# Kernel optimization log

Measured on AMD Instinct MI355X. Metric: run time of the kernel, lower is better.

The kernel has to match this reference:

```python
import jax, jax.numpy as jnp
import numpy as np

PS = 2      # patch_size
TOPK = 3    # topk


def setup_inputs() -> dict:
    key = jax.random.key(0)
    x = jax.random.normal(key, (16, 128, 64, 64), dtype=jnp.float32)
    alpha = jnp.asarray(5.0, dtype=jnp.float32)
    return {"x": x, "alpha": alpha}


def reference(x, alpha):
    ps = PS
    b, c, h, w = x.shape
    nph, npw = h // ps, w // ps
    npatch = nph * npw
    pa = ps * ps
    # F.normalize(x, p=2, dim=-3): L2-normalize over channels
    nrm = jnp.sqrt(jnp.sum(x * x, axis=1, keepdims=True))
    x = x / jnp.maximum(nrm, 1e-12)
    # patchify: [b,c,h,w] -> [b,c,num_patches,patch_area]
    x = x.reshape(b * c * nph, ps, npw, ps)
    x = jnp.swapaxes(x, 1, 2).reshape(b, c, npatch, pa)
    diag = np.arange(ps) * (ps + 1)          # diagonal positions within a patch
    x = x[:, :, :, diag]                     # [b,c,npatch,ps]
    x = jnp.swapaxes(x, 1, 3)                # [b,ps,npatch,c]
    # per-diagonal-pixel patch correlation matrix
    corr = jnp.einsum('bpnc,bpmc->bpnm', x, x)           # [b,ps,np,np]
    avg = jnp.mean(corr, axis=1, keepdims=True)
    corr = jnp.concatenate([corr, avg], axis=1)          # [b,ps+1,np,np]
    # gaussian self-suppression mask (1 - gaussian centered at each patch)
    rat_s = 0.05
    sr, sc = nph * rat_s, npw * rat_s
    ind_r = jnp.arange(nph, dtype=jnp.float32).reshape(1, nph, 1)
    ind_c = jnp.arange(npw, dtype=jnp.float32).reshape(1, 1, npw)
    cr, cc = jnp.meshgrid(jnp.arange(nph, dtype=jnp.float32),
                          jnp.arange(npw, dtype=jnp.float32), indexing='ij')
    cent_r = cr.reshape(npatch, 1, 1)
    cent_c = cc.reshape(npatch, 1, 1)
    g = jnp.exp(-(ind_r - cent_r) ** 2 / (2.0 * sr * sr)) \
        * jnp.exp(-(ind_c - cent_c) ** 2 / (2.0 * sc * sc))   # [np,nph,npw]
    mask = (1.0 - g).reshape(1, 1, npatch, npatch)
    s = (corr * mask) * alpha
    # dual (row + column) softmax
    a = jax.nn.softmax(s, axis=-1) * jax.nn.softmax(s, axis=-2)  # [b,ps+1,np,np]
    # scatter: diagonal in-patch pixels get their own map, rest get the avg map
    src = np.full(pa, ps, dtype=np.int64)
    src[diag] = np.arange(ps)
    a = a[:, src]                              # [b,pa,np,np]
    # un-patchify attention back to [b, npatch, h, w]
    a = jnp.swapaxes(a, 1, 3)                  # [b,np,np,pa]
    a = a.reshape(b * npatch * nph, npw, ps, ps)
    a = jnp.swapaxes(a, 1, 2)
    a = a.reshape(b, npatch, h, w)
    # top-k over the patch (correlation-source) dim
    vals = jax.lax.top_k(jnp.moveaxis(a, 1, -1), TOPK)[0]  # [b,h,w,k]
    return jnp.moveaxis(vals, -1, 1)           # [b,k,h,w]
```

## Files before the change

kernel.cpp:

```cpp
#include <hip/hip_runtime.h>
#include <math.h>

#define NB 16
#define NCH 128
#define NH 64
#define NW 64
#define NP 1024

#define TN 32
#define TM 128
#define KC 32
#define KP 36
#define PK 40

#define NTILE 144

typedef __attribute__((ext_vector_type(8))) short short8v;
typedef __attribute__((ext_vector_type(4))) float f32x4;

__device__ __forceinline__ float med3(float a, float b, float c) {
  return __builtin_amdgcn_fmed3f(a, b, c);
}
__device__ __forceinline__ void top3_ins(float& t0, float& t1, float& t2, float a) {
  float n0 = fmaxf(t0, a);
  float n1 = med3(a, t0, t1);
  float n2 = med3(a, t1, t2);
  t0 = n0; t1 = n1; t2 = n2;
}
__device__ __forceinline__ float dot4(float4 a, float4 b) {
  return a.x * b.x + a.y * b.y + a.z * b.z + a.w * b.w;
}
__device__ __forceinline__ ushort f2bf(float f) {
  unsigned u = __float_as_uint(f);
  unsigned r = (u + 0x7FFFu + ((u >> 16) & 1u)) >> 16;
  return (ushort)r;
}
__device__ __forceinline__ float bf2f(ushort h) {
  return __uint_as_float(((unsigned)h) << 16);
}

__global__ __launch_bounds__(256) void prep_split(const float* __restrict__ x,
                                                  ushort* __restrict__ Vs,
                                                  float* __restrict__ rsum) {
  int blk = blockIdx.x;
  int t = threadIdx.x;
  int gid = blk * 256 + t;
  if (gid < NB * 3 * NP) rsum[gid] = 0.f;

  int b = blk >> 5;
  int c = (blk >> 4) & 1;
  int ng = blk & 15;
  int nl = t >> 2;
  int kq = t & 3;
  int n = ng * 64 + nl;
  int i = 2 * (n >> 5) + c;
  int j = 2 * (n & 31) + c;
  const float* xp = x + (size_t)b * NCH * NH * NW + i * NW + j;

  float v[32];
#pragma unroll
  for (int e = 0; e < 32; ++e)
    v[e] = xp[(size_t)(kq * 32 + e) * NH * NW];

  float ss = 0.f;
#pragma unroll
  for (int e = 0; e < 32; ++e) ss += v[e] * v[e];
  ss += __shfl_xor(ss, 1, 64);
  ss += __shfl_xor(ss, 2, 64);
  float r = 1.0f / fmaxf(sqrtf(ss), 1e-12f);

  size_t base = ((size_t)(b * 2 + c) * 3) * NP * NCH + (size_t)n * NCH + kq * 32;
  ushort* p1 = Vs + base;
  ushort* p2 = Vs + base + (size_t)NP * NCH;
  ushort* p3 = Vs + base + (size_t)2 * NP * NCH;
#pragma unroll
  for (int kg2 = 0; kg2 < 4; ++kg2) {
    ushort h1[8], h2[8], h3[8];
#pragma unroll
    for (int e = 0; e < 8; ++e) {
      float vv = v[kg2 * 8 + e] * r;
      ushort a = f2bf(vv);
      float r1 = vv - bf2f(a);
      ushort bq = f2bf(r1);
      float r2 = r1 - bf2f(bq);
      ushort cq = f2bf(r2);
      h1[e] = a; h2[e] = bq; h3[e] = cq;
    }
    *(float4*)(p1 + kg2 * 8) = *(float4*)h1;
    *(float4*)(p2 + kg2 * 8) = *(float4*)h2;
    *(float4*)(p3 + kg2 * 8) = *(float4*)h3;
  }
}

__global__ __launch_bounds__(256, 4) void gemm_mfma(
    const ushort* __restrict__ Vs, const float* __restrict__ alpha_p,
    float2* __restrict__ Sbuf, float* __restrict__ rsum) {
  __shared__ __align__(16) char smem[3 * 32 * PK * 2 + 3 * 128 * PK * 2];
  ushort (*A_s)[32][PK] = reinterpret_cast<ushort(*)[32][PK]>(smem);
  ushort (*B_s)[128][PK] =
      reinterpret_cast<ushort(*)[128][PK]>(smem + 3 * 32 * PK * 2);
  float2 (*Ts)[33] = reinterpret_cast<float2(*)[33]>(smem);

  int wg = blockIdx.x;
  int xcd = wg & 7;
  int jj = wg >> 3;
  int half = (jj >= NTILE) ? 1 : 0;
  const int b = 2 * xcd + half;
  int id = jj - half * NTILE;
  int g = 0;
  while (id >= 4 * (8 - g)) { id -= 4 * (8 - g); ++g; }
  const int ni = 4 * g + id / (8 - g);
  const int mj = g + id % (8 - g);
  const int n0 = ni * TN;
  const int m0 = mj * TM;

  const int t = threadIdx.x;
  const int lane = t & 63, wv = t >> 6;
  const int jc = lane & 15, kg = lane >> 4;
  const float alpha = *alpha_p;
  const ushort* Vsb = Vs + (size_t)b * 6 * NP * NCH;
  float* rs = rsum + (size_t)b * 3 * NP;

  f32x4 acc[2][2][2];
#pragma unroll
  for (int c = 0; c < 2; ++c)
#pragma unroll
    for (int i = 0; i < 2; ++i)
#pragma unroll
      for (int j = 0; j < 2; ++j) acc[c][i][j] = (f32x4){0.f, 0.f, 0.f, 0.f};

#pragma unroll
  for (int c = 0; c < 2; ++c) {
    for (int k0 = 0; k0 < NCH; k0 += KC) {
      __syncthreads();
#pragma unroll
      for (int q = 0; q < 2; ++q) {
        int flat = q * 256 + t;
        if (flat < 384) {
          int p = flat >> 7;
          int rem = flat & 127;
          int row = rem >> 2, u = rem & 3;
          const ushort* src = Vsb + ((size_t)(c * 3 + p) * NP + n0 + row) * NCH + k0 + u * 8;
          *(float4*)&A_s[p][row][u * 8] = *(const float4*)src;
        }
      }
#pragma unroll
      for (int q = 0; q < 6; ++q) {
        int flat = q * 256 + t;
        int p = flat >> 9;
        int rem = flat & 511;
        int row = rem >> 2, u = rem & 3;
        const ushort* src = Vsb + ((size_t)(c * 3 + p) * NP + m0 + row) * NCH + k0 + u * 8;
        *(float4*)&B_s[p][row][u * 8] = *(const float4*)src;
      }
      __syncthreads();

      short8v a1n0 = *(const short8v*)&A_s[0][jc][kg * 8];
      short8v a1n1 = *(const short8v*)&A_s[0][16 + jc][kg * 8];
      short8v a2n0 = *(const short8v*)&A_s[1][jc][kg * 8];
      short8v a2n1 = *(const short8v*)&A_s[1][16 + jc][kg * 8];
      short8v a3n0 = *(const short8v*)&A_s[2][jc][kg * 8];
      short8v a3n1 = *(const short8v*)&A_s[2][16 + jc][kg * 8];
      {
        short8v b0 = *(const short8v*)&B_s[0][wv * 32 + jc][kg * 8];
        short8v b1 = *(const short8v*)&B_s[0][wv * 32 + 16 + jc][kg * 8];
        acc[c][0][0] = __builtin_amdgcn_mfma_f32_16x16x32_bf16(a1n0, b0, acc[c][0][0], 0, 0, 0);
        acc[c][1][0] = __builtin_amdgcn_mfma_f32_16x16x32_bf16(a1n1, b0, acc[c][1][0], 0, 0, 0);
        acc[c][0][1] = __builtin_amdgcn_mfma_f32_16x16x32_bf16(a1n0, b1, acc[c][0][1], 0, 0, 0);
        acc[c][1][1] = __builtin_amdgcn_mfma_f32_16x16x32_bf16(a1n1, b1, acc[c][1][1], 0, 0, 0);
        acc[c][0][0] = __builtin_amdgcn_mfma_f32_16x16x32_bf16(a2n0, b0, acc[c][0][0], 0, 0, 0);
        acc[c][1][0] = __builtin_amdgcn_mfma_f32_16x16x32_bf16(a2n1, b0, acc[c][1][0], 0, 0, 0);
        acc[c][0][1] = __builtin_amdgcn_mfma_f32_16x16x32_bf16(a2n0, b1, acc[c][0][1], 0, 0, 0);
        acc[c][1][1] = __builtin_amdgcn_mfma_f32_16x16x32_bf16(a2n1, b1, acc[c][1][1], 0, 0, 0);
        acc[c][0][0] = __builtin_amdgcn_mfma_f32_16x16x32_bf16(a3n0, b0, acc[c][0][0], 0, 0, 0);
        acc[c][1][0] = __builtin_amdgcn_mfma_f32_16x16x32_bf16(a3n1, b0, acc[c][1][0], 0, 0, 0);
        acc[c][0][1] = __builtin_amdgcn_mfma_f32_16x16x32_bf16(a3n0, b1, acc[c][0][1], 0, 0, 0);
        acc[c][1][1] = __builtin_amdgcn_mfma_f32_16x16x32_bf16(a3n1, b1, acc[c][1][1], 0, 0, 0);
      }
      {
        short8v b0 = *(const short8v*)&B_s[1][wv * 32 + jc][kg * 8];
        short8v b1 = *(const short8v*)&B_s[1][wv * 32 + 16 + jc][kg * 8];
        acc[c][0][0] = __builtin_amdgcn_mfma_f32_16x16x32_bf16(a1n0, b0, acc[c][0][0], 0, 0, 0);
        acc[c][1][0] = __builtin_amdgcn_mfma_f32_16x16x32_bf16(a1n1, b0, acc[c][1][0], 0, 0, 0);
        acc[c][0][1] = __builtin_amdgcn_mfma_f32_16x16x32_bf16(a1n0, b1, acc[c][0][1], 0, 0, 0);
        acc[c][1][1] = __builtin_amdgcn_mfma_f32_16x16x32_bf16(a1n1, b1, acc[c][1][1], 0, 0, 0);
        acc[c][0][0] = __builtin_amdgcn_mfma_f32_16x16x32_bf16(a2n0, b0, acc[c][0][0], 0, 0, 0);
        acc[c][1][0] = __builtin_amdgcn_mfma_f32_16x16x32_bf16(a2n1, b0, acc[c][1][0], 0, 0, 0);
        acc[c][0][1] = __builtin_amdgcn_mfma_f32_16x16x32_bf16(a2n0, b1, acc[c][0][1], 0, 0, 0);
        acc[c][1][1] = __builtin_amdgcn_mfma_f32_16x16x32_bf16(a2n1, b1, acc[c][1][1], 0, 0, 0);
      }
      {
        short8v b0 = *(const short8v*)&B_s[2][wv * 32 + jc][kg * 8];
        short8v b1 = *(const short8v*)&B_s[2][wv * 32 + 16 + jc][kg * 8];
        acc[c][0][0] = __builtin_amdgcn_mfma_f32_16x16x32_bf16(a1n0, b0, acc[c][0][0], 0, 0, 0);
        acc[c][1][0] = __builtin_amdgcn_mfma_f32_16x16x32_bf16(a1n1, b0, acc[c][1][0], 0, 0, 0);
        acc[c][0][1] = __builtin_amdgcn_mfma_f32_16x16x32_bf16(a1n0, b1, acc[c][0][1], 0, 0, 0);
        acc[c][1][1] = __builtin_amdgcn_mfma_f32_16x16x32_bf16(a1n1, b1, acc[c][1][1], 0, 0, 0);
      }
    }
  }

  __syncthreads();
  float e[2][4][3];
#pragma unroll
  for (int ns = 0; ns < 2; ++ns)
#pragma unroll
    for (int r = 0; r < 4; ++r)
#pragma unroll
      for (int c = 0; c < 3; ++c) e[ns][r][c] = 0.f;

#pragma unroll
  for (int ns = 0; ns < 2; ++ns) {
#pragma unroll
    for (int r = 0; r < 4; ++r) {
      int nl = ns * 16 + kg * 4 + r;
      int n = n0 + nl;
      int nr = n >> 5, nc = n & 31;
      float2* rowp = Sbuf + ((size_t)b * NP + n) * NP;
#pragma unroll
      for (int ms = 0; ms < 2; ++ms) {
        int ml = wv * 32 + ms * 16 + jc;
        int m = m0 + ml;
        int dr = nr - (m >> 5);
        int dc = nc - (m & 31);
        float gss = __expf(-(float)(dr * dr + dc * dc) * 0.1953125f);
        float wgt = (1.0f - gss) * alpha;
        float2 sv = make_float2(acc[0][ns][ms][r] * wgt, acc[1][ns][ms][r] * wgt);
        Ts[ml][nl] = sv;
        if (m >= n) {
          rowp[m] = sv;
          e[ns][r][0] += __expf(sv.x);
          e[ns][r][1] += __expf(sv.y);
          e[ns][r][2] += __expf(0.5f * (sv.x + sv.y));
        }
      }
    }
  }
#pragma unroll
  for (int off = 1; off < 16; off <<= 1) {
#pragma unroll
    for (int ns = 0; ns < 2; ++ns)
#pragma unroll
      for (int r = 0; r < 4; ++r)
#pragma unroll
        for (int c = 0; c < 3; ++c)
          e[ns][r][c] += __shfl_xor(e[ns][r][c], off, 64);
  }
  if (jc == 0) {
#pragma unroll
    for (int ns = 0; ns < 2; ++ns)
#pragma unroll
      for (int r = 0; r < 4; ++r)
#pragma unroll
        for (int c = 0; c < 3; ++c)
          atomicAdd(&rs[(size_t)c * NP + (n0 + ns * 16 + kg * 4 + r)], e[ns][r][c]);
  }

  __syncthreads();
#pragma unroll
  for (int q = 0; q < 16; ++q) {
    int flat = q * 256 + t;
    int ml = flat >> 5;
    int r = flat & 31;
    int m = m0 + ml;
    int n = n0 + r;
    if (m > n) Sbuf[((size_t)b * NP + m) * NP + n] = Ts[ml][r];
  }
  {
    int ml = t >> 1;
    int rh = (t & 1) * 16;
    int m = m0 + ml;
    float e0 = 0.f, e1 = 0.f, e2 = 0.f;
#pragma unroll
    for (int rr = 0; rr < 16; ++rr) {
      int r = rh + rr;
      int n = n0 + r;
      float2 sv = Ts[ml][r];
      if (m > n) {
        e0 += __expf(sv.x);
        e1 += __expf(sv.y);
        e2 += __expf(0.5f * (sv.x + sv.y));
      }
    }
    e0 += __shfl_xor(e0, 1, 64);
    e1 += __shfl_xor(e1, 1, 64);
    e2 += __shfl_xor(e2, 1, 64);
    if ((t & 1) == 0) {
      atomicAdd(&rs[(size_t)0 * NP + m], e0);
      atomicAdd(&rs[(size_t)1 * NP + m], e1);
      atomicAdd(&rs[(size_t)2 * NP + m], e2);
    }
  }
}

__global__ __launch_bounds__(256) void recip_kernel(float* __restrict__ p, int nelem) {
  int i = blockIdx.x * 256 + threadIdx.x;
  if (i < nelem) p[i] = 1.0f / p[i];
}

__global__ __launch_bounds__(256, 4) void topk_kernel(
    const float2* __restrict__ Sbuf, const float* __restrict__ rinv,
    float* __restrict__ out) {
  const int n = blockIdx.x, b = blockIdx.y;
  const int t = threadIdx.x;
  const float* rb = rinv + (size_t)b * 3 * NP;
  float rin[3];
#pragma unroll
  for (int c = 0; c < 3; ++c) rin[c] = rb[c * NP + n];
  const float2* row = Sbuf + ((size_t)b * NP + n) * NP;

  float t0[3] = {0.f, 0.f, 0.f}, t1[3] = {0.f, 0.f, 0.f}, t2[3] = {0.f, 0.f, 0.f};
#pragma unroll
  for (int q = 0; q < 4; ++q) {
    int m = t + q * 256;
    float2 s01 = row[m];
    float s[3];
    s[0] = s01.x; s[1] = s01.y; s[2] = 0.5f * (s01.x + s01.y);
#pragma unroll
    for (int c = 0; c < 3; ++c) {
      float a = __expf(2.0f * s[c]) * rin[c] * rb[c * NP + m];
      top3_ins(t0[c], t1[c], t2[c], a);
    }
  }
#pragma unroll
  for (int off = 1; off < 64; off <<= 1) {
#pragma unroll
    for (int c = 0; c < 3; ++c) {
      float o0 = __shfl_xor(t0[c], off, 64);
      float o1 = __shfl_xor(t1[c], off, 64);
      float o2 = __shfl_xor(t2[c], off, 64);
      top3_ins(t0[c], t1[c], t2[c], o0);
      top3_ins(t0[c], t1[c], t2[c], o1);
      top3_ins(t0[c], t1[c], t2[c], o2);
    }
  }
  __shared__ float lds[4][9];
  if ((t & 63) == 0) {
    int w = t >> 6;
#pragma unroll
    for (int c = 0; c < 3; ++c) {
      lds[w][c * 3 + 0] = t0[c];
      lds[w][c * 3 + 1] = t1[c];
      lds[w][c * 3 + 2] = t2[c];
    }
  }
  __syncthreads();
  if (t == 0) {
#pragma unroll
    for (int w = 1; w < 4; ++w)
#pragma unroll
      for (int c = 0; c < 3; ++c) {
        top3_ins(t0[c], t1[c], t2[c], lds[w][c * 3 + 0]);
        top3_ins(t0[c], t1[c], t2[c], lds[w][c * 3 + 1]);
        top3_ins(t0[c], t1[c], t2[c], lds[w][c * 3 + 2]);
      }
    int pr = n >> 5, pc = n & 31;
#pragma unroll
    for (int c = 0; c < 3; ++c) {
      int ii0, jj0, ii1 = -1, jj1 = -1;
      if (c == 0)      { ii0 = 2 * pr;     jj0 = 2 * pc; }
      else if (c == 1) { ii0 = 2 * pr + 1; jj0 = 2 * pc + 1; }
      else             { ii0 = 2 * pr;     jj0 = 2 * pc + 1;
                         ii1 = 2 * pr + 1; jj1 = 2 * pc; }
      out[(((size_t)b * 3 + 0) * NH + ii0) * NW + jj0] = t0[c];
      out[(((size_t)b * 3 + 1) * NH + ii0) * NW + jj0] = t1[c];
      out[(((size_t)b * 3 + 2) * NH + ii0) * NW + jj0] = t2[c];
      if (ii1 >= 0) {
        out[(((size_t)b * 3 + 0) * NH + ii1) * NW + jj1] = t0[c];
        out[(((size_t)b * 3 + 1) * NH + ii1) * NW + jj1] = t1[c];
        out[(((size_t)b * 3 + 2) * NH + ii1) * NW + jj1] = t2[c];
      }
    }
  }
}

__global__ __launch_bounds__(256) void prep_kernel(const float* __restrict__ x,
                                                   float* __restrict__ V) {
  int blk = blockIdx.x;
  int t = threadIdx.x;
  int b = blk >> 3;
  int c = (blk >> 2) & 1;
  int n = (blk & 3) * 256 + t;
  int i = 2 * (n >> 5) + c;
  int j = 2 * (n & 31) + c;
  const float* xp = x + (size_t)b * NCH * NH * NW + i * NW + j;
  float ss = 0.f;
#pragma unroll 8
  for (int ch = 0; ch < NCH; ++ch) {
    float v = xp[(size_t)ch * NH * NW];
    ss += v * v;
  }
  float r = 1.0f / fmaxf(sqrtf(ss), 1e-12f);
  float* vp = V + (((size_t)b * 2 + c) * NP + n) * NCH;
#pragma unroll 8
  for (int ch = 0; ch < NCH; ++ch) {
    vp[ch] = xp[(size_t)ch * NH * NW] * r;
  }
}

template <int PASS>
__global__ __launch_bounds__(256, 2) void corr_kernel(
    const float* __restrict__ V, const float* __restrict__ alpha_p,
    float* __restrict__ rsum_g, float* __restrict__ out) {
  __shared__ __align__(16) float As[2][TN][KP];
  __shared__ __align__(16) float Bs[2][TM][KP];

  const int b = blockIdx.y;
  const int n0 = blockIdx.x * TN;
  const int t = threadIdx.x;
  const int tx = t & 31;
  const int ty = t >> 5;
  const float alpha = *alpha_p;
  const float* Vb = V + (size_t)b * 2 * NP * NCH;

  float sm[3][4];
  float t0[3][4], t1[3][4], t2[3][4];
  float rin[3][4];
#pragma unroll
  for (int c = 0; c < 3; ++c)
#pragma unroll
    for (int i = 0; i < 4; ++i) {
      sm[c][i] = 0.f;
      t0[c][i] = 0.f; t1[c][i] = 0.f; t2[c][i] = 0.f;
    }
  if (PASS == 2) {
#pragma unroll
    for (int c = 0; c < 3; ++c)
#pragma unroll
      for (int i = 0; i < 4; ++i) {
        int n = n0 + ty * 4 + i;
        rin[c][i] = 1.0f / rsum_g[((size_t)b * 3 + c) * NP + n];
      }
  }

  for (int mc = 0; mc < NP / TM; ++mc) {
    const int m0 = mc * TM;
    float acc[2][4][4];
#pragma unroll
    for (int c = 0; c < 2; ++c)
#pragma unroll
      for (int i = 0; i < 4; ++i)
#pragma unroll
        for (int j = 0; j < 4; ++j) acc[c][i][j] = 0.f;

    for (int k0 = 0; k0 < NCH; k0 += KC) {
      __syncthreads();
#pragma unroll
      for (int q = 0; q < 2; ++q) {
        int flat = q * 256 + t;
        int c = flat >> 8;
        int rem = flat & 255;
        int row = rem >> 3;
        int kgx = rem & 7;
        float4 v4 = *(const float4*)(Vb + ((size_t)c * NP + n0 + row) * NCH + k0 + kgx * 4);
        *(float4*)&As[c][row][kgx * 4] = v4;
      }
#pragma unroll
      for (int q = 0; q < 8; ++q) {
        int flat = q * 256 + t;
        int c = flat >> 10;
        int rem = flat & 1023;
        int row = rem >> 3;
        int kgx = rem & 7;
        float4 v4 = *(const float4*)(Vb + ((size_t)c * NP + m0 + row) * NCH + k0 + kgx * 4);
        *(float4*)&Bs[c][row][kgx * 4] = v4;
      }
      __syncthreads();

      for (int kgx = 0; kgx < KC; kgx += 4) {
        float4 a4[2][4], b4[2][4];
#pragma unroll
        for (int c = 0; c < 2; ++c)
#pragma unroll
          for (int i = 0; i < 4; ++i)
            a4[c][i] = *(const float4*)&As[c][ty * 4 + i][kgx];
#pragma unroll
        for (int c = 0; c < 2; ++c)
#pragma unroll
          for (int j = 0; j < 4; ++j)
            b4[c][j] = *(const float4*)&Bs[c][tx + 32 * j][kgx];
#pragma unroll
        for (int c = 0; c < 2; ++c)
#pragma unroll
          for (int i = 0; i < 4; ++i)
#pragma unroll
            for (int j = 0; j < 4; ++j)
              acc[c][i][j] += dot4(a4[c][i], b4[c][j]);
      }
    }

    float rim[3][4];
    if (PASS == 2) {
#pragma unroll
      for (int c = 0; c < 3; ++c)
#pragma unroll
        for (int j = 0; j < 4; ++j) {
          int m = m0 + tx + 32 * j;
          rim[c][j] = 1.0f / rsum_g[((size_t)b * 3 + c) * NP + m];
        }
    }
#pragma unroll
    for (int i = 0; i < 4; ++i) {
      int n = n0 + ty * 4 + i;
      int nr = n >> 5, nc = n & 31;
      float s[3][4];
#pragma unroll
      for (int j = 0; j < 4; ++j) {
        int m = m0 + tx + 32 * j;
        int dr = nr - (m >> 5);
        int dc = nc - (m & 31);
        float gq = __expf(-(float)(dr * dr + dc * dc) * 0.1953125f);
        float wgt = (1.0f - gq) * alpha;
        float s0v = acc[0][i][j] * wgt;
        float s1v = acc[1][i][j] * wgt;
        s[0][j] = s0v; s[1][j] = s1v; s[2][j] = 0.5f * (s0v + s1v);
      }
      if (PASS == 1) {
#pragma unroll
        for (int c = 0; c < 3; ++c) {
          sm[c][i] += __expf(s[c][0]) + __expf(s[c][1]) +
                      __expf(s[c][2]) + __expf(s[c][3]);
        }
      } else {
#pragma unroll
        for (int c = 0; c < 3; ++c) {
#pragma unroll
          for (int j = 0; j < 4; ++j) {
            float a = __expf(2.0f * s[c][j]) * rin[c][i] * rim[c][j];
            top3_ins(t0[c][i], t1[c][i], t2[c][i], a);
          }
        }
      }
    }
  }

  if (PASS == 1) {
#pragma unroll
    for (int off = 1; off < 32; off <<= 1) {
#pragma unroll
      for (int c = 0; c < 3; ++c)
#pragma unroll
        for (int i = 0; i < 4; ++i)
          sm[c][i] += __shfl_xor(sm[c][i], off, 64);
    }
    if (tx == 0) {
#pragma unroll
      for (int c = 0; c < 3; ++c)
#pragma unroll
        for (int i = 0; i < 4; ++i) {
          int n = n0 + ty * 4 + i;
          rsum_g[((size_t)b * 3 + c) * NP + n] = sm[c][i];
        }
    }
  } else {
#pragma unroll
    for (int off = 1; off < 32; off <<= 1) {
#pragma unroll
      for (int c = 0; c < 3; ++c)
#pragma unroll
        for (int i = 0; i < 4; ++i) {
          float o0 = __shfl_xor(t0[c][i], off, 64);
          float o1 = __shfl_xor(t1[c][i], off, 64);
          float o2 = __shfl_xor(t2[c][i], off, 64);
          top3_ins(t0[c][i], t1[c][i], t2[c][i], o0);
          top3_ins(t0[c][i], t1[c][i], t2[c][i], o1);
          top3_ins(t0[c][i], t1[c][i], t2[c][i], o2);
        }
    }
    if (tx == 0) {
#pragma unroll
      for (int c = 0; c < 3; ++c)
#pragma unroll
        for (int i = 0; i < 4; ++i) {
          int n = n0 + ty * 4 + i;
          int pr = n >> 5, pc = n & 31;
          float v0 = t0[c][i], v1 = t1[c][i], v2 = t2[c][i];
          int ii0, jj0, ii1 = -1, jj1 = -1;
          if (c == 0)      { ii0 = 2 * pr;     jj0 = 2 * pc; }
          else if (c == 1) { ii0 = 2 * pr + 1; jj0 = 2 * pc + 1; }
          else             { ii0 = 2 * pr;     jj0 = 2 * pc + 1;
                             ii1 = 2 * pr + 1; jj1 = 2 * pc; }
          out[(((size_t)b * 3 + 0) * NH + ii0) * NW + jj0] = v0;
          out[(((size_t)b * 3 + 1) * NH + ii0) * NW + jj0] = v1;
          out[(((size_t)b * 3 + 2) * NH + ii0) * NW + jj0] = v2;
          if (ii1 >= 0) {
            out[(((size_t)b * 3 + 0) * NH + ii1) * NW + jj1] = v0;
            out[(((size_t)b * 3 + 1) * NH + ii1) * NW + jj1] = v1;
            out[(((size_t)b * 3 + 2) * NH + ii1) * NW + jj1] = v2;
          }
        }
    }
  }
}

extern "C" void kernel_launch(void* const* d_in, const int* in_sizes, int n_in,
                              void* d_out, int out_size, void* d_ws, size_t ws_size,
                              hipStream_t stream) {
  const float* x = (const float*)d_in[0];
  const float* alpha = (const float*)d_in[1];
  float* out = (float*)d_out;

  const size_t nVsU = (size_t)NB * 6 * NP * NCH;
  const size_t nRs = (size_t)NB * 3 * NP;
  const size_t nS = (size_t)NB * NP * NP;

  ushort* Vs = (ushort*)d_ws;
  float* rsum = (float*)(Vs + nVsU);
  float2* Sbuf = (float2*)(rsum + nRs);

  const size_t need_bytes = nVsU * 2 + nRs * 4 + nS * 8;

  if (ws_size >= need_bytes) {
    prep_split<<<512, 256, 0, stream>>>(x, Vs, rsum);
    gemm_mfma<<<NTILE * NB, 256, 0, stream>>>(Vs, alpha, Sbuf, rsum);
    recip_kernel<<<(NB * 3 * NP + 255) / 256, 256, 0, stream>>>(rsum, NB * 3 * NP);
    topk_kernel<<<dim3(NP, NB), 256, 0, stream>>>(Sbuf, rsum, out);
  } else {
    float* V = (float*)d_ws;
    float* rsum_f = V + (size_t)NB * 2 * NP * NCH;
    prep_kernel<<<128, 256, 0, stream>>>(x, V);
    corr_kernel<1><<<dim3(NP / TN, NB), 256, 0, stream>>>(V, alpha, rsum_f, out);
    corr_kernel<2><<<dim3(NP / TN, NB), 256, 0, stream>>>(V, alpha, rsum_f, out);
  }
}
```

Before: 148.4 us.

## Store symmetric score tiles once and do per-tile partial top-k with merge

The GEMM kernel now writes each upper-triangular 32x128 score tile once in tile-major order, instead of writing both the tile and its mirrored transpose into a full dense NP×NP buffer. Column exp-sums are now reduced in registers with shuffles rather than through an LDS transpose, which removes two barriers. A new tile_topk kernel reads each tile once and computes partial top-3 values for both its rows and its columns. A merge kernel then combines these partials per patch. This roughly halves the score-matrix traffic written and read through HBM, at the cost of an extra launch and scattered partial reads in the merge.

```diff
diff --git a/kernel.cpp b/kernel.cpp
--- a/kernel.cpp
+++ b/kernel.cpp
@@ -37,6 +37,9 @@
 }
 __device__ __forceinline__ float bf2f(ushort h) {
   return __uint_as_float(((unsigned)h) << 16);
+}
+__device__ __forceinline__ int tile_base(int g) {
+  return 32 * g - 2 * g * (g - 1);
 }
 
 __global__ __launch_bounds__(256) void prep_split(const float* __restrict__ x,
@@ -99,7 +102,6 @@
   ushort (*A_s)[32][PK] = reinterpret_cast<ushort(*)[32][PK]>(smem);
   ushort (*B_s)[128][PK] =
       reinterpret_cast<ushort(*)[128][PK]>(smem + 3 * 32 * PK * 2);
-  float2 (*Ts)[33] = reinterpret_cast<float2(*)[33]>(smem);
 
   int wg = blockIdx.x;
   int xcd = wg & 7;
@@ -107,6 +109,7 @@
   int half = (jj >= NTILE) ? 1 : 0;
   const int b = 2 * xcd + half;
   int id = jj - half * NTILE;
+  const int tid0 = id;
   int g = 0;
   while (id >= 4 * (8 - g)) { id -= 4 * (8 - g); ++g; }
   const int ni = 4 * g + id / (8 - g);
@@ -200,14 +203,18 @@
     }
   }
 
-  __syncthreads();
   float e[2][4][3];
+  float gcol[2][3];
 #pragma unroll
   for (int ns = 0; ns < 2; ++ns)
 #pragma unroll
     for (int r = 0; r < 4; ++r)
 #pragma unroll
       for (int c = 0; c < 3; ++c) e[ns][r][c] = 0.f;
+#pragma unroll
+  for (int ms = 0; ms < 2; ++ms)
+#pragma unroll
+    for (int c = 0; c < 3; ++c) gcol[ms][c] = 0.f;
 
 #pragma unroll
   for (int ns = 0; ns < 2; ++ns) {
@@ -216,7 +223,7 @@
       int nl = ns * 16 + kg * 4 + r;
       int n = n0 + nl;
       int nr = n >> 5, nc = n & 31;
-      float2* rowp = Sbuf + ((size_t)b * NP + n) * NP;
+      float2* rowp = Sbuf + ((size_t)(b * NTILE + tid0) * 32 + nl) * TM;
 #pragma unroll
       for (int ms = 0; ms < 2; ++ms) {
         int ml = wv * 32 + ms * 16 + jc;
@@ -225,14 +232,16 @@
         int dc = nc - (m & 31);
         float gss = __expf(-(float)(dr * dr + dc * dc) * 0.1953125f);
         float wgt = (1.0f - gss) * alpha;
-        float2 sv = make_float2(acc[0][ns][ms][r] * wgt, acc[1][ns][ms][r] * wgt);
-        Ts[ml][nl] = sv;
+        float s0 = acc[0][ns][ms][r] * wgt;
+        float s1 = acc[1][ns][ms][r] * wgt;
+        float e0 = __expf(s0);
+        float e1 = __expf(s1);
+        float e2 = __expf(0.5f * (s0 + s1));
         if (m >= n) {
-          rowp[m] = sv;
-          e[ns][r][0] += __expf(sv.x);
-          e[ns][r][1] += __expf(sv.y);
-          e[ns][r][2] += __expf(0.5f * (sv.x + sv.y));
+          rowp[ml] = make_float2(s0, s1);
+          e[ns][r][0] += e0; e[ns][r][1] += e1; e[ns][r][2] += e2;
         }
+        if (m > n) { gcol[ms][0] += e0; gcol[ms][1] += e1; gcol[ms][2] += e2; }
       }
     }
   }
@@ -255,40 +264,21 @@
         for (int c = 0; c < 3; ++c)
           atomicAdd(&rs[(size_t)c * NP + (n0 + ns * 16 + kg * 4 + r)], e[ns][r][c]);
   }
-
-  __syncthreads();
-#pragma unroll
-  for (int q = 0; q < 16; ++q) {
-    int flat = q * 256 + t;
-    int ml = flat >> 5;
-    int r = flat & 31;
-    int m = m0 + ml;
-    int n = n0 + r;
-    if (m > n) Sbuf[((size_t)b * NP + m) * NP + n] = Ts[ml][r];
-  }
-  {
-    int ml = t >> 1;
-    int rh = (t & 1) * 16;
-    int m = m0 + ml;
-    float e0 = 0.f, e1 = 0.f, e2 = 0.f;
-#pragma unroll
-    for (int rr = 0; rr < 16; ++rr) {
-      int r = rh + rr;
-      int n = n0 + r;
-      float2 sv = Ts[ml][r];
-      if (m > n) {
-        e0 += __expf(sv.x);
-        e1 += __expf(sv.y);
-        e2 += __expf(0.5f * (sv.x + sv.y));
-      }
-    }
-    e0 += __shfl_xor(e0, 1, 64);
-    e1 += __shfl_xor(e1, 1, 64);
-    e2 += __shfl_xor(e2, 1, 64);
-    if ((t & 1) == 0) {
-      atomicAdd(&rs[(size_t)0 * NP + m], e0);
-      atomicAdd(&rs[(size_t)1 * NP + m], e1);
-      atomicAdd(&rs[(size_t)2 * NP + m], e2);
+#pragma unroll
+  for (int off = 16; off < 64; off <<= 1) {
+#pragma unroll
+    for (int ms = 0; ms < 2; ++ms)
+#pragma unroll
+      for (int c = 0; c < 3; ++c)
+        gcol[ms][c] += __shfl_xor(gcol[ms][c], off, 64);
+  }
+  if (kg == 0) {
+#pragma unroll
+    for (int ms = 0; ms < 2; ++ms) {
+      int m = m0 + wv * 32 + ms * 16 + jc;
+#pragma unroll
+      for (int c = 0; c < 3; ++c)
+        atomicAdd(&rs[(size_t)c * NP + m], gcol[ms][c]);
     }
   }
 }
@@ -298,79 +288,165 @@
   if (i < nelem) p[i] = 1.0f / p[i];
 }
 
-__global__ __launch_bounds__(256, 4) void topk_kernel(
+__global__ __launch_bounds__(256, 4) void tile_topk(
     const float2* __restrict__ Sbuf, const float* __restrict__ rinv,
-    float* __restrict__ out) {
-  const int n = blockIdx.x, b = blockIdx.y;
+    float* __restrict__ P) {
+  __shared__ float2 tile[32][129];
+
+  const int b = blockIdx.y;
+  int id = blockIdx.x;
+  const int tid0 = id;
+  int g = 0;
+  while (id >= 4 * (8 - g)) { id -= 4 * (8 - g); ++g; }
+  const int ni = 4 * g + id / (8 - g);
+  const int mj = g + id % (8 - g);
+  const int n0 = ni * TN;
+  const int m0 = mj * TM;
+
   const int t = threadIdx.x;
   const float* rb = rinv + (size_t)b * 3 * NP;
-  float rin[3];
-#pragma unroll
-  for (int c = 0; c < 3; ++c) rin[c] = rb[c * NP + n];
-  const float2* row = Sbuf + ((size_t)b * NP + n) * NP;
-
-  float t0[3] = {0.f, 0.f, 0.f}, t1[3] = {0.f, 0.f, 0.f}, t2[3] = {0.f, 0.f, 0.f};
-#pragma unroll
-  for (int q = 0; q < 4; ++q) {
-    int m = t + q * 256;
-    float2 s01 = row[m];
-    float s[3];
-    s[0] = s01.x; s[1] = s01.y; s[2] = 0.5f * (s01.x + s01.y);
+  const float2* src = Sbuf + (size_t)(b * NTILE + tid0) * 32 * TM;
+  float* Pp = P + ((size_t)(b * NTILE + tid0) * 160) * 9;
+
+#pragma unroll
+  for (int q = 0; q < 16; ++q) {
+    int flat = q * 256 + t;
+    int row = flat >> 7;
+    int colu = flat & 127;
+    tile[row][colu] = src[row * TM + colu];
+  }
+  __syncthreads();
+
+  {
+    int rl = t >> 3;
+    int c0 = (t & 7) * 16;
+    int n = n0 + rl;
+    float rin0 = rb[(size_t)0 * NP + n];
+    float rin1 = rb[(size_t)1 * NP + n];
+    float rin2 = rb[(size_t)2 * NP + n];
+    float t0[3] = {0.f, 0.f, 0.f}, t1[3] = {0.f, 0.f, 0.f}, t2[3] = {0.f, 0.f, 0.f};
+#pragma unroll
+    for (int cc = 0; cc < 16; ++cc) {
+      int ml = c0 + cc;
+      int m = m0 + ml;
+      if (m >= n) {
+        float2 sv = tile[rl][ml];
+        float a0 = __expf(2.0f * sv.x) * rin0 * rb[(size_t)0 * NP + m];
+        float a1 = __expf(2.0f * sv.y) * rin1 * rb[(size_t)1 * NP + m];
+        float a2 = __expf(sv.x + sv.y) * rin2 * rb[(size_t)2 * NP + m];
+        top3_ins(t0[0], t1[0], t2[0], a0);
+        top3_ins(t0[1], t1[1], t2[1], a1);
+        top3_ins(t0[2], t1[2], t2[2], a2);
+      }
+    }
+#pragma unroll
+    for (int off = 1; off < 8; off <<= 1) {
+#pragma unroll
+      for (int c = 0; c < 3; ++c) {
+        float o0 = __shfl_xor(t0[c], off, 64);
+        float o1 = __shfl_xor(t1[c], off, 64);
+        float o2 = __shfl_xor(t2[c], off, 64);
+        top3_ins(t0[c], t1[c], t2[c], o0);
+        top3_ins(t0[c], t1[c], t2[c], o1);
+        top3_ins(t0[c], t1[c], t2[c], o2);
+      }
+    }
+    if ((t & 7) == 0) {
+#pragma unroll
+      for (int c = 0; c < 3; ++c) {
+        Pp[(size_t)rl * 9 + c * 3 + 0] = t0[c];
+        Pp[(size_t)rl * 9 + c * 3 + 1] = t1[c];
+        Pp[(size_t)rl * 9 + c * 3 + 2] = t2[c];
+      }
+    }
+  }
+
+  {
+    int cu = t >> 1;
+    int r0 = (t & 1) * 16;
+    int m = m0 + cu;
+    float rim0 = rb[(size_t)0 * NP + m];
+    float rim1 = rb[(size_t)1 * NP + m];
+    float rim2 = rb[(size_t)2 * NP + m];
+    float t0[3] = {0.f, 0.f, 0.f}, t1[3] = {0.f, 0.f, 0.f}, t2[3] = {0.f, 0.f, 0.f};
+#pragma unroll
+    for (int rr = 0; rr < 16; ++rr) {
+      int row = r0 + rr;
+      int n = n0 + row;
+      if (n < m) {
+        float2 sv = tile[row][cu];
+        float a0 = __expf(2.0f * sv.x) * rim0 * rb[(size_t)0 * NP + n];
+        float a1 = __expf(2.0f * sv.y) * rim1 * rb[(size_t)1 * NP + n];
+        float a2 = __expf(sv.x + sv.y) * rim2 * rb[(size_t)2 * NP + n];
+        top3_ins(t0[0], t1[0], t2[0], a0);
+        top3_ins(t0[1], t1[1], t2[1], a1);
+        top3_ins(t0[2], t1[2], t2[2], a2);
+      }
+    }
 #pragma unroll
     for (int c = 0; c < 3; ++c) {
-      float a = __expf(2.0f * s[c]) * rin[c] * rb[c * NP + m];
-      top3_ins(t0[c], t1[c], t2[c], a);
-    }
-  }
-#pragma unroll
-  for (int off = 1; off < 64; off <<= 1) {
-#pragma unroll
-    for (int c = 0; c < 3; ++c) {
-      float o0 = __shfl_xor(t0[c], off, 64);
-      float o1 = __shfl_xor(t1[c], off, 64);
-      float o2 = __shfl_xor(t2[c], off, 64);
+      float o0 = __shfl_xor(t0[c], 1, 64);
+      float o1 = __shfl_xor(t1[c], 1, 64);
+      float o2 = __shfl_xor(t2[c], 1, 64);
       top3_ins(t0[c], t1[c], t2[c], o0);
       top3_ins(t0[c], t1[c], t2[c], o1);
       top3_ins(t0[c], t1[c], t2[c], o2);
     }
-  }
-  __shared__ float lds[4][9];
-  if ((t & 63) == 0) {
-    int w = t >> 6;
-#pragma unroll
-    for (int c = 0; c < 3; ++c) {
-      lds[w][c * 3 + 0] = t0[c];
-      lds[w][c * 3 + 1] = t1[c];
-      lds[w][c * 3 + 2] = t2[c];
-    }
-  }
-  __syncthreads();
-  if (t == 0) {
-#pragma unroll
-    for (int w = 1; w < 4; ++w)
+    if ((t & 1) == 0) {
 #pragma unroll
       for (int c = 0; c < 3; ++c) {
-        top3_ins(t0[c], t1[c], t2[c], lds[w][c * 3 + 0]);
-        top3_ins(t0[c], t1[c], t2[c], lds[w][c * 3 + 1]);
-        top3_ins(t0[c], t1[c], t2[c], lds[w][c * 3 + 2]);
-      }
-    int pr = n >> 5, pc = n & 31;
-#pragma unroll
-    for (int c = 0; c < 3; ++c) {
-      int ii0, jj0, ii1 = -1, jj1 = -1;
-      if (c == 0)      { ii0 = 2 * pr;     jj0 = 2 * pc; }
-      else if (c == 1) { ii0 = 2 * pr + 1; jj0 = 2 * pc + 1; }
-      else             { ii0 = 2 * pr;     jj0 = 2 * pc + 1;
-                         ii1 = 2 * pr + 1; jj1 = 2 * pc; }
-      out[(((size_t)b * 3 + 0) * NH + ii0) * NW + jj0] = t0[c];
-      out[(((size_t)b * 3 + 1) * NH + ii0) * NW + jj0] = t1[c];
-      out[(((size_t)b * 3 + 2) * NH + ii0) * NW + jj0] = t2[c];
-      if (ii1 >= 0) {
-        out[(((size_t)b * 3 + 0) * NH + ii1) * NW + jj1] = t0[c];
-        out[(((size_t)b * 3 + 1) * NH + ii1) * NW + jj1] = t1[c];
-        out[(((size_t)b * 3 + 2) * NH + ii1) * NW + jj1] = t2[c];
-      }
-    }
+        Pp[(size_t)(32 + cu) * 9 + c * 3 + 0] = t0[c];
+        Pp[(size_t)(32 + cu) * 9 + c * 3 + 1] = t1[c];
+        Pp[(size_t)(32 + cu) * 9 + c * 3 + 2] = t2[c];
+      }
+    }
+  }
+}
+
+__global__ __launch_bounds__(256) void merge_kernel(
+    const float* __restrict__ P, float* __restrict__ out) {
+  int gid = blockIdx.x * 256 + threadIdx.x;
+  int n = gid & (NP - 1);
+  int tmp = gid >> 10;
+  int c = tmp % 3;
+  int b = tmp / 3;
+
+  const float* Pb = P + (size_t)b * NTILE * 160 * 9;
+  int g = n >> 7;
+  int ni = n >> 5;
+  int nl = n & 31;
+  int ml = n & 127;
+
+  float u0 = 0.f, u1 = 0.f, u2 = 0.f;
+  int rbase = tile_base(g) + (ni - 4 * g) * (8 - g) - g;
+  for (int mj = g; mj < 8; ++mj) {
+    const float* p = Pb + ((size_t)(rbase + mj) * 160 + nl) * 9 + c * 3;
+    top3_ins(u0, u1, u2, p[0]);
+    top3_ins(u0, u1, u2, p[1]);
+    top3_ins(u0, u1, u2, p[2]);
+  }
+  for (int nii = 0; nii <= 4 * g + 3; ++nii) {
+    int gg = nii >> 2;
+    int tid = tile_base(gg) + (nii - 4 * gg) * (8 - gg) + (g - gg);
+    const float* p = Pb + ((size_t)tid * 160 + 32 + ml) * 9 + c * 3;
+    top3_ins(u0, u1, u2, p[0]);
+    top3_ins(u0, u1, u2, p[1]);
+    top3_ins(u0, u1, u2, p[2]);
+  }
+
+  int pr = n >> 5, pc = n & 31;
+  int ii0, jj0, ii1 = -1, jj1 = -1;
+  if (c == 0)      { ii0 = 2 * pr;     jj0 = 2 * pc; }
+  else if (c == 1) { ii0 = 2 * pr + 1; jj0 = 2 * pc + 1; }
+  else             { ii0 = 2 * pr;     jj0 = 2 * pc + 1;
+                     ii1 = 2 * pr + 1; jj1 = 2 * pc; }
+  out[(((size_t)b * 3 + 0) * NH + ii0) * NW + jj0] = u0;
+  out[(((size_t)b * 3 + 1) * NH + ii0) * NW + jj0] = u1;
+  out[(((size_t)b * 3 + 2) * NH + ii0) * NW + jj0] = u2;
+  if (ii1 >= 0) {
+    out[(((size_t)b * 3 + 0) * NH + ii1) * NW + jj1] = u0;
+    out[(((size_t)b * 3 + 1) * NH + ii1) * NW + jj1] = u1;
+    out[(((size_t)b * 3 + 2) * NH + ii1) * NW + jj1] = u2;
   }
 }
 
@@ -602,19 +678,22 @@
 
   const size_t nVsU = (size_t)NB * 6 * NP * NCH;
   const size_t nRs = (size_t)NB * 3 * NP;
-  const size_t nS = (size_t)NB * NP * NP;
+  const size_t nSbuf = (size_t)NB * NTILE * 32 * TM;
+  const size_t nP = (size_t)NB * NTILE * 160 * 9;
 
   ushort* Vs = (ushort*)d_ws;
   float* rsum = (float*)(Vs + nVsU);
   float2* Sbuf = (float2*)(rsum + nRs);
-
-  const size_t need_bytes = nVsU * 2 + nRs * 4 + nS * 8;
+  float* P = (float*)(Sbuf + nSbuf);
+
+  const size_t need_bytes = nVsU * 2 + nRs * 4 + nSbuf * 8 + nP * 4;
 
   if (ws_size >= need_bytes) {
     prep_split<<<512, 256, 0, stream>>>(x, Vs, rsum);
     gemm_mfma<<<NTILE * NB, 256, 0, stream>>>(Vs, alpha, Sbuf, rsum);
     recip_kernel<<<(NB * 3 * NP + 255) / 256, 256, 0, stream>>>(rsum, NB * 3 * NP);
-    topk_kernel<<<dim3(NP, NB), 256, 0, stream>>>(Sbuf, rsum, out);
+    tile_topk<<<dim3(NTILE, NB), 256, 0, stream>>>(Sbuf, rsum, P);
+    merge_kernel<<<(NB * 3 * NP) / 256, 256, 0, stream>>>(P, out);
   } else {
     float* V = (float*)d_ws;
     float* rsum_f = V + (size_t)NB * 2 * NP * NCH;
```

Result: slower. 161.4 us (+8.8%).
